# Kernel optimization log

Measured on AMD Instinct MI355X. Metric: run time of the kernel, lower is better.

The kernel has to match this reference:

```python
import jax, jax.numpy as jnp
import numpy as np

B, S, D, H = 2, 2048, 1024, 16
HD = D // H
SPARSITY = 0.1
LAMBDA_MAX = 10.0
ALPHA = 5.0


def local_prior_mask(seq_len: int, sparsity: float) -> jnp.ndarray:
    # |i - j| <= window_size // 2, window_size = int(seq_len * sparsity)
    window_size = max(1, int(seq_len * sparsity))
    rows = jnp.arange(seq_len)[:, None]
    cols = jnp.arange(seq_len)[None, :]
    return jnp.abs(rows - cols) <= (window_size // 2)


def setup_inputs() -> dict:
    key = jax.random.key(0)
    ks = jax.random.split(key, 12)
    scale = 1.0 / np.sqrt(D)
    inp = {
        'x': jax.random.normal(ks[0], (B, S, D), dtype=jnp.float32),
        'u_prev': jax.random.uniform(ks[1], (B, 1), dtype=jnp.float32),
        'Wq': jax.random.normal(ks[2], (D, D), dtype=jnp.float32) * scale,
        'bq': jnp.zeros((D,), dtype=jnp.float32),
        'Wk': jax.random.normal(ks[3], (D, D), dtype=jnp.float32) * scale,
        'bk': jnp.zeros((D,), dtype=jnp.float32),
        'Wv': jax.random.normal(ks[4], (D, D), dtype=jnp.float32) * scale,
        'bv': jnp.zeros((D,), dtype=jnp.float32),
        'Wo': jax.random.normal(ks[5], (D, D), dtype=jnp.float32) * scale,
        'bo': jnp.zeros((D,), dtype=jnp.float32),
    }
    return inp


def reference(x, u_prev, Wq, bq, Wk, bk, Wv, bv, Wo, bo):
    b, s, _ = x.shape
    # projections (torch Linear: y = x W^T + b)
    def proj(W, bias):
        return (x @ W.T + bias).reshape(b, s, H, HD).transpose(0, 2, 1, 3)  # [B,H,S,HD]
    q = proj(Wq, bq)
    k = proj(Wk, bk)
    v = proj(Wv, bv)

    # dynamic gating: lambda = lambda_max * exp(-alpha * u_prev), shape [B,1,1,1]
    lam = (LAMBDA_MAX * jnp.exp(-ALPHA * u_prev)).reshape(b, 1, 1, 1)

    prior = local_prior_mask(s, SPARSITY)  # [S,S] bool

    scores = jnp.einsum('bhqd,bhkd->bhqk', q, k) / jnp.sqrt(jnp.asarray(HD, x.dtype))
    # additive prior bias: penalize positions outside the structural prior by -lambda
    scores = scores - lam * (~prior).astype(x.dtype)

    attn = jax.nn.softmax(scores, axis=-1)
    out = jnp.einsum('bhqk,bhkd->bhqd', attn, v)           # [B,H,S,HD]
    out = out.transpose(0, 2, 1, 3).reshape(b, s, D)        # [B,S,D]
    out = out @ Wo.T + bo
    return out, lam.reshape(b, 1)
```

## Files before the change

### kernel.cpp

```cpp
#include <hip/hip_runtime.h>

typedef __attribute__((ext_vector_type(8))) short short8;
typedef __attribute__((ext_vector_type(4))) float f32x4;

#define MFMA16(a,b,c) __builtin_amdgcn_mfma_f32_16x16x32_bf16(a,b,c,0,0,0)

__device__ __forceinline__ unsigned short f2bf(float f){
  unsigned int u = __float_as_uint(f);
  u += 0x7FFF + ((u>>16)&1);
  return (unsigned short)(u>>16);
}

__device__ __forceinline__ float fexp2(float x){
#if __has_builtin(__builtin_amdgcn_exp2f)
  return __builtin_amdgcn_exp2f(x);
#else
  return exp2f(x);
#endif
}

__device__ __forceinline__ void gl_lds16(const void* g, void* l){
  __builtin_amdgcn_global_load_lds((const __attribute__((address_space(1))) void*)g,
                                   (__attribute__((address_space(3))) void*)l, 16, 0, 0);
}

__global__ void prep_k(const float* __restrict__ x,
                       const float* __restrict__ Wq, const float* __restrict__ Wk,
                       const float* __restrict__ Wv, const float* __restrict__ Wo,
                       const float* __restrict__ u,
                       unsigned short* __restrict__ xb,
                       unsigned short* __restrict__ Wqkvb,
                       unsigned short* __restrict__ Wob,
                       float* __restrict__ out){
  const int bid = blockIdx.x;
  const float* src;
  unsigned short* dst;
  int lb;
  if (bid < 4096)      { src = x;  dst = xb;              lb = bid; }
  else if (bid < 5120) { src = Wq; dst = Wqkvb;           lb = bid - 4096; }
  else if (bid < 6144) { src = Wk; dst = Wqkvb + 1048576; lb = bid - 5120; }
  else if (bid < 7168) { src = Wv; dst = Wqkvb + 2097152; lb = bid - 6144; }
  else                 { src = Wo; dst = Wob;             lb = bid - 7168; }
  const int i = (lb*256 + threadIdx.x)*4;
  float4 v = *(const float4*)(src + i);
  ushort4 o;
  o.x = f2bf(v.x); o.y = f2bf(v.y); o.z = f2bf(v.z); o.w = f2bf(v.w);
  *(ushort4*)(dst + i) = o;
  if (bid == 0 && threadIdx.x < 2)
    out[4194304 + threadIdx.x] = 10.f*__expf(-5.f*u[threadIdx.x]);
}

template<int MODE>
__global__ __launch_bounds__(256) void gemm_bt(
  const unsigned short* __restrict__ A,
  const unsigned short* __restrict__ Bw,
  const float* __restrict__ bias0, const float* __restrict__ bias1, const float* __restrict__ bias2,
  unsigned short* __restrict__ Qo, unsigned short* __restrict__ Ko, unsigned short* __restrict__ VTo,
  float* __restrict__ Co,
  int M, int N, int K)
{
  __shared__ unsigned short As[2][128*32];
  __shared__ unsigned short Bs[2][128*32];
  const int tid = threadIdx.x;
  const int m0 = blockIdx.y*128, n0 = blockIdx.x*128;
  const int w = tid>>6, lane = tid&63, lr = lane&15, lg = lane>>4;
  const int wm = w>>1, wn = w&1;
  const int nk = K/32;

  auto stage = [&](int buf, int kt){
    const unsigned short* Ag = A + (size_t)m0*K + kt*32;
    const unsigned short* Bg = Bw + (size_t)n0*K + kt*32;
    #pragma unroll
    for (int it=0; it<2; ++it){
      int slot = it*256 + tid;
      gl_lds16(Ag + (size_t)(slot>>2)*K + (slot&3)*8, &As[buf][slot*8]);
    }
    #pragma unroll
    for (int it=0; it<2; ++it){
      int slot = it*256 + tid;
      gl_lds16(Bg + (size_t)(slot>>2)*K + (slot&3)*8, &Bs[buf][slot*8]);
    }
  };

  f32x4 acc[4][4] = {};
  stage(0,0);
  for (int kt=0; kt<nk; ++kt){
    int cur = kt&1;
    __syncthreads();
    if (kt+1 < nk) stage(cur^1, kt+1);
    short8 af[4], bfr[4];
    #pragma unroll
    for (int i=0;i<4;++i) af[i]  = *(const short8*)&As[cur][(wm*64 + i*16 + lr)*32 + lg*8];
    #pragma unroll
    for (int j=0;j<4;++j) bfr[j] = *(const short8*)&Bs[cur][(wn*64 + j*16 + lr)*32 + lg*8];
    #pragma unroll
    for (int i=0;i<4;++i)
      #pragma unroll
      for (int j=0;j<4;++j)
        acc[i][j] = MFMA16(af[i], bfr[j], acc[i][j]);
  }

  #pragma unroll
  for (int i=0;i<4;++i){
    #pragma unroll
    for (int j=0;j<4;++j){
      const int n  = n0 + wn*64 + j*16 + lr;
      const int mb = m0 + wm*64 + i*16 + lg*4;
      if (MODE==0){
        const int which = n>>10, nn = n&1023;
        const float bv = (which==0) ? bias0[nn] : (which==1) ? bias1[nn] : bias2[nn];
        const int h = nn>>6, hd = nn&63;
        #pragma unroll
        for (int r=0;r<4;++r){
          const int m = mb + r;
          const int b = m>>11, s = m&2047;
          const unsigned short u = f2bf(acc[i][j][r] + bv);
          const size_t bh = (size_t)(b*16 + h);
          if (which==0)      Qo[(bh*2048 + s)*64 + hd] = u;
          else if (which==1) Ko[(bh*2048 + s)*64 + hd] = u;
          else               VTo[(bh*64 + hd)*2048 + s] = u;
        }
      } else {
        const float bv = bias0[n];
        #pragma unroll
        for (int r=0;r<4;++r){
          const int m = mb + r;
          Co[(size_t)m*N + n] = acc[i][j][r] + bv;
        }
      }
    }
  }
}

__global__ __launch_bounds__(256, 4) void attn_k(
  const unsigned short* __restrict__ Qb,
  const unsigned short* __restrict__ Kb,
  const unsigned short* __restrict__ VT,
  const float* __restrict__ u_prev,
  unsigned short* __restrict__ Out)
{
  const int lin = blockIdx.x + (blockIdx.y << 5);
  const int f   = ((lin & 7) << 7) + (lin >> 3);
  const int qt  = f & 31, bh = f >> 5;
  const int b = bh>>4, h = bh&15;
  const float lam = 10.f * __expf(-5.f * u_prev[b]);
  const float nlamb = -lam * 1.4426950408889634f;
  const int tid = threadIdx.x;
  const int w = tid>>6, lane = tid&63, lr = lane&15, lg = lane>>4;
  const int q0 = qt*64 + w*16;

  const unsigned short* Qp = Qb + (size_t)bh*2048*64;
  const unsigned short* Kp = Kb + (size_t)bh*2048*64;
  const unsigned short* Vp = VT + (size_t)bh*64*2048;

  __shared__ unsigned short Ks[3][2048];
  __shared__ unsigned short Vs[3][2048];
  __shared__ unsigned short p_lds[4][16][40];

  const unsigned short* ksrc = Kp + (tid&31)*64 + (tid>>5)*8;
  const unsigned short* vsrc = Vp + (size_t)(tid&63)*2048 + (tid>>6)*8;
  unsigned short* kd0 = &Ks[0][tid*8];
  unsigned short* kd1 = &Ks[1][tid*8];
  unsigned short* kd2 = &Ks[2][tid*8];
  unsigned short* vd0 = &Vs[0][tid*8];
  unsigned short* vd1 = &Vs[1][tid*8];
  unsigned short* vd2 = &Vs[2][tid*8];

  const unsigned short* kf0p = &Ks[0][(lg*32+lr)*8];
  const unsigned short* kf1p = &Ks[1][(lg*32+lr)*8];
  const unsigned short* kf2p = &Ks[2][(lg*32+lr)*8];
  const unsigned short* vf0p = &Vs[0][(lg*64+lr)*8];
  const unsigned short* vf1p = &Vs[1][(lg*64+lr)*8];
  const unsigned short* vf2p = &Vs[2][(lg*64+lr)*8];
  const unsigned short* pap  = &p_lds[w][lr][lg*8];
  unsigned short* pwp = &p_lds[w][lg*4][lr];

  short8 qf0 = *(const short8*)&Qp[(size_t)(q0+lr)*64 +      lg*8];
  short8 qf1 = *(const short8*)&Qp[(size_t)(q0+lr)*64 + 32 + lg*8];

  const float c1 = 0.18033688011112042f;
  float l_run[4] = {0.f, 0.f, 0.f, 0.f};
  f32x4 o0 = {}, o1 = {}, o2 = {}, o3 = {};
  const f32x4 zf = {};
  f32x4 sA0, sA1, sB0, sB1, sC0, sC1;

#define STAGE_(KD, VD, KT) do{ const int kw_ = (KT)&63; \
    gl_lds16(ksrc + ((size_t)kw_<<11), (KD)); \
    gl_lds16(vsrc + (kw_<<5), (VD)); }while(0)

#define BAR_ do{ \
    asm volatile("s_waitcnt vmcnt(2) lgkmcnt(0)\n\ts_barrier" ::: "memory"); \
    __builtin_amdgcn_sched_barrier(0); }while(0)

#define QKM_(KP, S0, S1) do{ \
    short8 ka_ = *(const short8*)(KP); \
    short8 kb_ = *(const short8*)((KP)+1024); \
    short8 kc_ = *(const short8*)((KP)+128); \
    short8 kd_ = *(const short8*)((KP)+1152); \
    S0 = MFMA16(qf0, ka_, zf); S0 = MFMA16(qf1, kb_, S0); \
    S1 = MFMA16(qf0, kc_, zf); S1 = MFMA16(qf1, kd_, S1); }while(0)

#define SOFT_(KT, SIN0, SIN1) do{ \
    const int k0_ = (KT)*32; \
    const int cls_ = (k0_ > q0 + 117 || k0_ < q0 - 133) ? 2 \
                   : (k0_ >= q0 - 87 && k0_ <= q0 + 71) ? 0 : 1; \
    _Pragma("unroll") \
    for (int r=0;r<4;++r){ \
      const int qi_ = q0 + lg*4 + r; \
      float b0 = 0.f, b1 = 0.f; \
      if (cls_ == 2){ b0 = nlamb; b1 = nlamb; } \
      else if (cls_ == 1){ \
        int d0 = qi_ - (k0_ + lr);      if (d0<0) d0 = -d0; \
        int d1 = qi_ - (k0_ + 16 + lr); if (d1<0) d1 = -d1; \
        if (d0 > 102) b0 = nlamb; \
        if (d1 > 102) b1 = nlamb; \
      } \
      const float p0 = fexp2(fmaf((SIN0)[r], c1, b0)); \
      const float p1 = fexp2(fmaf((SIN1)[r], c1, b1)); \
      l_run[r] += p0 + p1; \
      pwp[r*40]      = (unsigned short)(__float_as_uint(p0)>>16); \
      pwp[r*40 + 16] = (unsigned short)(__float_as_uint(p1)>>16); \
    } }while(0)

#define BODY_(KT, VFPC, KDC, VDC, KFPN, SIN0, SIN1, SOUT0, SOUT1) do{ \
    SOFT_((KT), SIN0, SIN1); \
    short8 vfa_ = *(const short8*)(VFPC); \
    short8 vfb_ = *(const short8*)((VFPC)+128); \
    short8 vfc_ = *(const short8*)((VFPC)+256); \
    short8 vfd_ = *(const short8*)((VFPC)+384); \
    short8 pa_  = *(const short8*)(pap); \
    BAR_; \
    STAGE_((KDC), (VDC), (KT)+3); \
    QKM_((KFPN), SOUT0, SOUT1); \
    o0 = MFMA16(pa_, vfa_, o0); \
    o1 = MFMA16(pa_, vfb_, o1); \
    o2 = MFMA16(pa_, vfc_, o2); \
    o3 = MFMA16(pa_, vfd_, o3); }while(0)

  STAGE_(kd0, vd0, 0);
  STAGE_(kd1, vd1, 1);
  STAGE_(kd2, vd2, 2);
  BAR_;
  QKM_(kf0p, sA0, sA1);

  for (int it=0; it<21; ++it){
    const int kt = it*3;
    BODY_(kt,   vf0p, kd0, vd0, kf1p, sA0, sA1, sB0, sB1);
    BODY_(kt+1, vf1p, kd1, vd1, kf2p, sB0, sB1, sC0, sC1);
    BODY_(kt+2, vf2p, kd2, vd2, kf0p, sC0, sC1, sA0, sA1);
  }
  {
    SOFT_(63, sA0, sA1);
    short8 vfa_ = *(const short8*)(vf0p);
    short8 vfb_ = *(const short8*)(vf0p+128);
    short8 vfc_ = *(const short8*)(vf0p+256);
    short8 vfd_ = *(const short8*)(vf0p+384);
    asm volatile("s_waitcnt lgkmcnt(0)" ::: "memory");
    __builtin_amdgcn_sched_barrier(0);
    short8 pa_  = *(const short8*)(pap);
    o0 = MFMA16(pa_, vfa_, o0);
    o1 = MFMA16(pa_, vfb_, o1);
    o2 = MFMA16(pa_, vfc_, o2);
    o3 = MFMA16(pa_, vfd_, o3);
  }
#undef BODY_
#undef SOFT_
#undef QKM_
#undef BAR_
#undef STAGE_

  #pragma unroll
  for (int off=1; off<16; off<<=1)
    #pragma unroll
    for (int r=0;r<4;++r)
      l_run[r] += __shfl_xor(l_run[r], off, 64);

  #pragma unroll
  for (int r=0;r<4;++r){
    const int qi = q0 + lg*4 + r;
    const float linv = 1.0f / l_run[r];
    unsigned short* op = &Out[((size_t)b*2048 + qi)*1024 + h*64 + lr];
    op[0]  = f2bf(o0[r] * linv);
    op[16] = f2bf(o1[r] * linv);
    op[32] = f2bf(o2[r] * linv);
    op[48] = f2bf(o3[r] * linv);
  }
}

extern "C" void kernel_launch(void* const* d_in, const int* in_sizes, int n_in,
                              void* d_out, int out_size, void* d_ws, size_t ws_size,
                              hipStream_t stream){
  const float* x  = (const float*)d_in[0];
  const float* u  = (const float*)d_in[1];
  const float* Wq = (const float*)d_in[2];
  const float* bq = (const float*)d_in[3];
  const float* Wk = (const float*)d_in[4];
  const float* bk = (const float*)d_in[5];
  const float* Wv = (const float*)d_in[6];
  const float* bv = (const float*)d_in[7];
  const float* Wo = (const float*)d_in[8];
  const float* bo = (const float*)d_in[9];
  float* out = (float*)d_out;

  unsigned char* ws = (unsigned char*)d_ws;
  unsigned short* xb    = (unsigned short*)(ws);
  unsigned short* attnb = xb;
  unsigned short* Wqkvb = (unsigned short*)(ws + 8388608);
  unsigned short* Wob   = (unsigned short*)(ws + 14680064);
  unsigned short* Qb2   = (unsigned short*)(ws + 16777216);
  unsigned short* Kb2   = (unsigned short*)(ws + 25165824);
  unsigned short* VTb   = (unsigned short*)(ws + 33554432);

  prep_k<<<8192, 256, 0, stream>>>(x, Wq, Wk, Wv, Wo, u, xb, Wqkvb, Wob, out);

  gemm_bt<0><<<dim3(24,32), 256, 0, stream>>>(xb, Wqkvb, bq, bk, bv,
                                              Qb2, Kb2, VTb, nullptr, 4096, 3072, 1024);
  attn_k<<<dim3(32,32), 256, 0, stream>>>(Qb2, Kb2, VTb, u, attnb);
  gemm_bt<1><<<dim3(8,32), 256, 0, stream>>>(attnb, Wob, bo, nullptr, nullptr,
                                             nullptr, nullptr, nullptr, out, 4096, 1024, 1024);
}
```

Before: 143.2 us.

## Software-pipeline softmax after PV MFMAs with triple-buffered P tiles; swizzle GEMM blocks

The attention loop is reordered so the softmax for the next key tile runs after the current PV MFMAs are issued, rather than before the barrier. The P tile in LDS is triple-buffered so this cross-iteration overlap is safe, and the rotating score registers shrink to one pair. Separately, the GEMM kernel remaps block indices with a stride-8 swizzle to change the tile visit order for cache locality. This adds LDS use for P and depends on the compiler overlapping the exp/VALU work with MFMA latency.

```diff
diff --git a/kernel.cpp b/kernel.cpp
--- a/kernel.cpp
+++ b/kernel.cpp
@@ -62,7 +62,11 @@
   __shared__ unsigned short As[2][128*32];
   __shared__ unsigned short Bs[2][128*32];
   const int tid = threadIdx.x;
-  const int m0 = blockIdx.y*128, n0 = blockIdx.x*128;
+  const int nbx = gridDim.x;
+  const int lin = blockIdx.x + blockIdx.y*nbx;
+  const int cpx = (nbx*gridDim.y) >> 3;
+  const int fsw = (lin & 7)*cpx + (lin >> 3);
+  const int m0 = (fsw/nbx)*128, n0 = (fsw%nbx)*128;
   const int w = tid>>6, lane = tid&63, lr = lane&15, lg = lane>>4;
   const int wm = w>>1, wn = w&1;
   const int nk = K/32;
@@ -155,7 +159,7 @@
 
   __shared__ unsigned short Ks[3][2048];
   __shared__ unsigned short Vs[3][2048];
-  __shared__ unsigned short p_lds[4][16][40];
+  __shared__ unsigned short p_lds[4][3][16][40];
 
   const unsigned short* ksrc = Kp + (tid&31)*64 + (tid>>5)*8;
   const unsigned short* vsrc = Vp + (size_t)(tid&63)*2048 + (tid>>6)*8;
@@ -172,8 +176,8 @@
   const unsigned short* vf0p = &Vs[0][(lg*64+lr)*8];
   const unsigned short* vf1p = &Vs[1][(lg*64+lr)*8];
   const unsigned short* vf2p = &Vs[2][(lg*64+lr)*8];
-  const unsigned short* pap  = &p_lds[w][lr][lg*8];
-  unsigned short* pwp = &p_lds[w][lg*4][lr];
+  const unsigned short* pap  = &p_lds[w][0][lr][lg*8];
+  unsigned short* pwp = &p_lds[w][0][lg*4][lr];
 
   short8 qf0 = *(const short8*)&Qp[(size_t)(q0+lr)*64 +      lg*8];
   short8 qf1 = *(const short8*)&Qp[(size_t)(q0+lr)*64 + 32 + lg*8];
@@ -182,7 +186,7 @@
   float l_run[4] = {0.f, 0.f, 0.f, 0.f};
   f32x4 o0 = {}, o1 = {}, o2 = {}, o3 = {};
   const f32x4 zf = {};
-  f32x4 sA0, sA1, sB0, sB1, sC0, sC1;
+  f32x4 s0, s1;
 
 #define STAGE_(KD, VD, KT) do{ const int kw_ = (KT)&63; \
     gl_lds16(ksrc + ((size_t)kw_<<11), (KD)); \
@@ -192,15 +196,15 @@
     asm volatile("s_waitcnt vmcnt(2) lgkmcnt(0)\n\ts_barrier" ::: "memory"); \
     __builtin_amdgcn_sched_barrier(0); }while(0)
 
-#define QKM_(KP, S0, S1) do{ \
+#define QKM_(KP) do{ \
     short8 ka_ = *(const short8*)(KP); \
     short8 kb_ = *(const short8*)((KP)+1024); \
     short8 kc_ = *(const short8*)((KP)+128); \
     short8 kd_ = *(const short8*)((KP)+1152); \
-    S0 = MFMA16(qf0, ka_, zf); S0 = MFMA16(qf1, kb_, S0); \
-    S1 = MFMA16(qf0, kc_, zf); S1 = MFMA16(qf1, kd_, S1); }while(0)
-
-#define SOFT_(KT, SIN0, SIN1) do{ \
+    s0 = MFMA16(qf0, ka_, zf); s0 = MFMA16(qf1, kb_, s0); \
+    s1 = MFMA16(qf0, kc_, zf); s1 = MFMA16(qf1, kd_, s1); }while(0)
+
+#define SOFT_(KT, PWOFF) do{ \
     const int k0_ = (KT)*32; \
     const int cls_ = (k0_ > q0 + 117 || k0_ < q0 - 133) ? 2 \
                    : (k0_ >= q0 - 87 && k0_ <= q0 + 71) ? 0 : 1; \
@@ -215,49 +219,47 @@
         if (d0 > 102) b0 = nlamb; \
         if (d1 > 102) b1 = nlamb; \
       } \
-      const float p0 = fexp2(fmaf((SIN0)[r], c1, b0)); \
-      const float p1 = fexp2(fmaf((SIN1)[r], c1, b1)); \
+      const float p0 = fexp2(fmaf(s0[r], c1, b0)); \
+      const float p1 = fexp2(fmaf(s1[r], c1, b1)); \
       l_run[r] += p0 + p1; \
-      pwp[r*40]      = (unsigned short)(__float_as_uint(p0)>>16); \
-      pwp[r*40 + 16] = (unsigned short)(__float_as_uint(p1)>>16); \
+      pwp[(PWOFF) + r*40]      = (unsigned short)(__float_as_uint(p0)>>16); \
+      pwp[(PWOFF) + r*40 + 16] = (unsigned short)(__float_as_uint(p1)>>16); \
     } }while(0)
 
-#define BODY_(KT, VFPC, KDC, VDC, KFPN, SIN0, SIN1, SOUT0, SOUT1) do{ \
-    SOFT_((KT), SIN0, SIN1); \
+#define BODY_(KT, VFPC, KDC, VDC, KFPN, PROFF, PWOFF) do{ \
+    short8 pa_  = *(const short8*)(pap + (PROFF)); \
     short8 vfa_ = *(const short8*)(VFPC); \
     short8 vfb_ = *(const short8*)((VFPC)+128); \
     short8 vfc_ = *(const short8*)((VFPC)+256); \
     short8 vfd_ = *(const short8*)((VFPC)+384); \
-    short8 pa_  = *(const short8*)(pap); \
     BAR_; \
     STAGE_((KDC), (VDC), (KT)+3); \
-    QKM_((KFPN), SOUT0, SOUT1); \
+    QKM_((KFPN)); \
     o0 = MFMA16(pa_, vfa_, o0); \
     o1 = MFMA16(pa_, vfb_, o1); \
     o2 = MFMA16(pa_, vfc_, o2); \
-    o3 = MFMA16(pa_, vfd_, o3); }while(0)
+    o3 = MFMA16(pa_, vfd_, o3); \
+    SOFT_((KT)+1, PWOFF); }while(0)
 
   STAGE_(kd0, vd0, 0);
   STAGE_(kd1, vd1, 1);
   STAGE_(kd2, vd2, 2);
   BAR_;
-  QKM_(kf0p, sA0, sA1);
+  QKM_(kf0p);
+  SOFT_(0, 0);
 
   for (int it=0; it<21; ++it){
     const int kt = it*3;
-    BODY_(kt,   vf0p, kd0, vd0, kf1p, sA0, sA1, sB0, sB1);
-    BODY_(kt+1, vf1p, kd1, vd1, kf2p, sB0, sB1, sC0, sC1);
-    BODY_(kt+2, vf2p, kd2, vd2, kf0p, sC0, sC1, sA0, sA1);
+    BODY_(kt,   vf0p, kd0, vd0, kf1p, 0,    640);
+    BODY_(kt+1, vf1p, kd1, vd1, kf2p, 640,  1280);
+    BODY_(kt+2, vf2p, kd2, vd2, kf0p, 1280, 0);
   }
   {
-    SOFT_(63, sA0, sA1);
+    short8 pa_  = *(const short8*)(pap);
     short8 vfa_ = *(const short8*)(vf0p);
     short8 vfb_ = *(const short8*)(vf0p+128);
     short8 vfc_ = *(const short8*)(vf0p+256);
     short8 vfd_ = *(const short8*)(vf0p+384);
-    asm volatile("s_waitcnt lgkmcnt(0)" ::: "memory");
-    __builtin_amdgcn_sched_barrier(0);
-    short8 pa_  = *(const short8*)(pap);
     o0 = MFMA16(pa_, vfa_, o0);
     o1 = MFMA16(pa_, vfb_, o1);
     o2 = MFMA16(pa_, vfc_, o2);
```

After: 144.3 us. About the same (+0.8%).

## Stage V-transpose epilogue through LDS and swizzle GEMM block order

Applied to the files above, without the earlier changes.

For the V slice of the fused QKV projection, the accumulator tile is written transposed into shared memory and then stored to the V^T buffer as 16-byte rows along the sequence dimension, replacing scattered 2-byte strided stores. The block index is also remapped so consecutive blocks are spread across eight groups, which is meant to improve L2/cache locality or XCD distribution. The LDS staging adds two barriers per half-tile and reuses the operand buffers after the main loop.

```diff
diff --git a/kernel.cpp b/kernel.cpp
--- a/kernel.cpp
+++ b/kernel.cpp
@@ -59,10 +59,15 @@
   float* __restrict__ Co,
   int M, int N, int K)
 {
-  __shared__ unsigned short As[2][128*32];
-  __shared__ unsigned short Bs[2][128*32];
+  __shared__ unsigned short SM[2][2][128*32];
+  unsigned short (*As)[128*32] = SM[0];
+  unsigned short (*Bs)[128*32] = SM[1];
   const int tid = threadIdx.x;
-  const int m0 = blockIdx.y*128, n0 = blockIdx.x*128;
+  const int nbx = gridDim.x;
+  const int lin = blockIdx.x + blockIdx.y*nbx;
+  const int cpx = (nbx*gridDim.y) >> 3;
+  const int fsw = (lin & 7)*cpx + (lin >> 3);
+  const int m0 = (fsw/nbx)*128, n0 = (fsw%nbx)*128;
   const int w = tid>>6, lane = tid&63, lr = lane&15, lg = lane>>4;
   const int wm = w>>1, wn = w&1;
   const int nk = K/32;
@@ -100,6 +105,43 @@
         acc[i][j] = MFMA16(af[i], bfr[j], acc[i][j]);
   }
 
+  if (MODE==0 && (n0>>10)==2){
+    unsigned short (*Ct)[136] = (unsigned short(*)[136])&SM[0][0][0];
+    const int nb = n0 - 2048;
+    #pragma unroll
+    for (int hh=0; hh<2; ++hh){
+      __syncthreads();
+      if (wn == hh){
+        #pragma unroll
+        for (int i=0;i<4;++i)
+          #pragma unroll
+          for (int j=0;j<4;++j){
+            const int nl = j*16 + lr;
+            const float bv = bias2[nb + hh*64 + nl];
+            ushort4 pk;
+            pk.x = f2bf(acc[i][j][0] + bv);
+            pk.y = f2bf(acc[i][j][1] + bv);
+            pk.z = f2bf(acc[i][j][2] + bv);
+            pk.w = f2bf(acc[i][j][3] + bv);
+            *(ushort4*)&Ct[nl][wm*64 + i*16 + lg*4] = pk;
+          }
+      }
+      __syncthreads();
+      #pragma unroll
+      for (int it=0; it<4; ++it){
+        const int idx = it*256 + tid;
+        const int nl = idx >> 4, mc = idx & 15;
+        short8 vv = *(const short8*)&Ct[nl][mc*8];
+        const int nn = nb + hh*64 + nl;
+        const int h = nn>>6, hd = nn&63;
+        const int mg = m0 + mc*8;
+        const int b = mg>>11, s = mg&2047;
+        *(short8*)&VTo[((size_t)(b*16 + h)*64 + hd)*2048 + s] = vv;
+      }
+    }
+    return;
+  }
+
   #pragma unroll
   for (int i=0;i<4;++i){
     #pragma unroll
@@ -108,7 +150,7 @@
       const int mb = m0 + wm*64 + i*16 + lg*4;
       if (MODE==0){
         const int which = n>>10, nn = n&1023;
-        const float bv = (which==0) ? bias0[nn] : (which==1) ? bias1[nn] : bias2[nn];
+        const float bv = (which==0) ? bias0[nn] : bias1[nn];
         const int h = nn>>6, hd = nn&63;
         #pragma unroll
         for (int r=0;r<4;++r){
@@ -116,9 +158,8 @@
           const int b = m>>11, s = m&2047;
           const unsigned short u = f2bf(acc[i][j][r] + bv);
           const size_t bh = (size_t)(b*16 + h);
-          if (which==0)      Qo[(bh*2048 + s)*64 + hd] = u;
-          else if (which==1) Ko[(bh*2048 + s)*64 + hd] = u;
-          else               VTo[(bh*64 + hd)*2048 + s] = u;
+          if (which==0) Qo[(bh*2048 + s)*64 + hd] = u;
+          else          Ko[(bh*2048 + s)*64 + hd] = u;
         }
       } else {
         const float bv = bias0[n];
```

Result: faster. 140.1 us, median of 3 (-2.2%).
